# Performance work log

Hardware: AMD Instinct MI355X
Metric: run time of the kernel (lower is better)

Reference implementation:

```python
import jax, jax.numpy as jnp
import numpy as np

MARGIN = 0.5  # init kwarg 'margin'
TWO_N, D = 8192, 256


def setup_inputs() -> dict:
    key = jax.random.key(0)
    k1, k2 = jax.random.split(key)
    embeddings = jax.random.normal(k1, (TWO_N, D), dtype=jnp.float32)
    neg_mask = jax.random.bernoulli(k2, 0.5, (TWO_N, TWO_N))  # bool [2N, 2N]
    return {"embeddings": embeddings, "neg_mask": neg_mask}


def _cdist(x, y):
    # Euclidean pairwise distances via the Gram trick (matches torch.cdist p=2)
    x2 = jnp.sum(x * x, axis=-1)[:, None]
    y2 = jnp.sum(y * y, axis=-1)[None, :]
    sq = jnp.maximum(x2 + y2 - 2.0 * (x @ y.T), 0.0)
    return jnp.sqrt(sq + 1e-12)


def reference(embeddings, neg_mask):
    two_n = embeddings.shape[0]
    n = two_n // 2
    d = _cdist(embeddings, embeddings)  # [2N, 2N]
    # masked sum of exp(margin - d) per anchor row (vectorizes the python loop)
    exp_neg = jnp.where(neg_mask, jnp.exp(MARGIN - d), 0.0)
    row_sums = exp_neg.sum(axis=1)  # [2N]
    idx = jnp.arange(n)
    ap = d[idx, idx + n]  # anchor-positive distances [N]
    j = jnp.log(row_sums[:n] + row_sums[n:]) + ap  # [N]
    # original skips NaN entries before the mean
    valid = ~jnp.isnan(j)
    r2 = jnp.where(valid, jnp.square(jnp.maximum(j, 0.0)), 0.0)
    cnt = jnp.maximum(valid.sum(), 1).astype(r2.dtype)
    loss = r2.sum() / cnt / 2.0
    return loss
```

## Files before the change

### kernel.cpp

```cpp
#include <hip/hip_runtime.h>
#include <hip/hip_bf16.h>
#include <stdint.h>

#define TWO_N  8192
#define NHALF  4096
#define DDIM   256
#define MARGIN 0.5f
#define NTRI   2080

static const size_t OFF_EMB  = 0;
static const size_t OFF_X2   = 4u * 1024 * 1024;
static const size_t OFF_AP   = OFF_X2 + (size_t)TWO_N * 4;
static const size_t OFF_FLAG = OFF_AP + (size_t)NHALF * 4;
static const size_t OFF_BITM = 5u * 1024 * 1024;
static const size_t OFF_RS   = 13u * 1024 * 1024;

typedef __attribute__((ext_vector_type(8))) short bf16x8;
typedef __attribute__((ext_vector_type(4))) float f32x4;

__device__ inline ushort f2bf(float f) {
  uint32_t u = __float_as_uint(f);
  uint32_t r = (u + 0x7FFFu + ((u >> 16) & 1u)) >> 16;
  return (ushort)r;
}
__device__ inline float bf2f(ushort h) { return __uint_as_float((uint32_t)h << 16); }

__device__ inline void gload_lds4(const void* g, void* l) {
  __builtin_amdgcn_global_load_lds(
      (const __attribute__((address_space(1))) uint32_t*)(uintptr_t)g,
      (__attribute__((address_space(3))) uint32_t*)(uint32_t)(uintptr_t)l,
      4, 0, 0);
}

__global__ __launch_bounds__(256) void smv2_prep(
    const float* __restrict__ emb,
    const uint32_t* __restrict__ maskw,
    ushort* __restrict__ emb_bf,
    float* __restrict__ x2,
    int* __restrict__ flag)
{
  const int t = threadIdx.x;
  if (blockIdx.x == 0) {
    __shared__ int sflag;
    if (t == 0) sflag = 0;
    __syncthreads();
    int found = 0;
    #pragma unroll
    for (int k = 0; k < 8; ++k) {
      uint32_t w = maskw[t * 8 + k];
      if (w > 1u && (w & 0xFEFEFEFEu) == 0u) found = 1;
    }
    if (found) atomicOr(&sflag, 1);
    __syncthreads();
    if (t == 0) *flag = sflag;
  }
  const int row  = blockIdx.x * 8 + (t >> 5);
  const int lane = t & 31;
  const float* rp = emb + (size_t)row * DDIM + lane * 8;
  float4 v0 = *(const float4*)(rp);
  float4 v1 = *(const float4*)(rp + 4);
  float vals[8] = {v0.x, v0.y, v0.z, v0.w, v1.x, v1.y, v1.z, v1.w};
  uint32_t packed[4];
  float ss = 0.f;
  #pragma unroll
  for (int k = 0; k < 4; ++k) {
    ushort h0 = f2bf(vals[2 * k]);
    ushort h1 = f2bf(vals[2 * k + 1]);
    packed[k] = (uint32_t)h0 | ((uint32_t)h1 << 16);
    float f0 = bf2f(h0), f1 = bf2f(h1);
    ss += f0 * f0 + f1 * f1;
  }
  *(uint4*)(emb_bf + (size_t)row * DDIM + lane * 8) =
      make_uint4(packed[0], packed[1], packed[2], packed[3]);
  #pragma unroll
  for (int m = 1; m < 32; m <<= 1) ss += __shfl_xor(ss, m);
  if (lane == 0) x2[row] = ss;
}

__global__ __launch_bounds__(256) void smv2_pack(
    const uint8_t* __restrict__ mask8,
    const int* __restrict__ flagp,
    uint32_t* __restrict__ bitM,
    float* __restrict__ rs)
{
  const int t = threadIdx.x;
  if (blockIdx.x == 0) {
    float4 z = {0.f, 0.f, 0.f, 0.f};
    #pragma unroll
    for (int i = 0; i < 8; ++i) ((float4*)rs)[t * 8 + i] = z;
  }
  const int tid = blockIdx.x * 256 + t;
  const int isByte = *flagp;
  if (isByte) {
    #pragma unroll
    for (int it = 0; it < 4; ++it) {
      const int idx = it * (2048 * 256) + tid;
      const uint4 a = ((const uint4*)mask8)[(size_t)idx * 2];
      const uint4 b = ((const uint4*)mask8)[(size_t)idx * 2 + 1];
      const uint32_t wsv[8] = {a.x, a.y, a.z, a.w, b.x, b.y, b.z, b.w};
      uint32_t out = 0;
      #pragma unroll
      for (int j = 0; j < 8; ++j)
        out |= ((((wsv[j] & 0x01010101u) * 0x01020408u) >> 24) & 0xFu) << (4 * j);
      bitM[idx] = out;
    }
  } else {
    const uint32_t* maskw = (const uint32_t*)mask8;
    #pragma unroll
    for (int it = 0; it < 4; ++it) {
      const int idx = it * (2048 * 256) + tid;
      uint32_t out = 0;
      #pragma unroll
      for (int j = 0; j < 8; ++j) {
        const uint4 wv = ((const uint4*)maskw)[(size_t)idx * 8 + j];
        out |= (wv.x != 0u ? 1u : 0u) << (4 * j);
        out |= (wv.y != 0u ? 1u : 0u) << (4 * j + 1);
        out |= (wv.z != 0u ? 1u : 0u) << (4 * j + 2);
        out |= (wv.w != 0u ? 1u : 0u) << (4 * j + 3);
      }
      bitM[idx] = out;
    }
  }
}

__global__ __launch_bounds__(512, 6) void smv2_main(
    const ushort* __restrict__ emb_bf,
    const float* __restrict__ x2,
    const uint8_t* __restrict__ bitM,
    float* __restrict__ ap,
    float* __restrict__ rs)
{
  __shared__ uint32_t ldsM[512];
  __shared__ float ldsX[256];
  __shared__ float part[512];
  __shared__ float part2[256];

  const int t = threadIdx.x;

  const int bid = blockIdx.x;
  const int idx = (bid & 7) * (NTRI / 8) + (bid >> 3);
  float rf = sqrtf(8.f * (float)idx + 1.f);
  int bx = (int)((rf - 1.f) * 0.5f);
  while ((bx + 1) * (bx + 2) / 2 <= idx) ++bx;
  while (bx * (bx + 1) / 2 > idx) --bx;
  const int by = idx - bx * (bx + 1) / 2;
  const int brow = by * 128;
  const int bcol = bx * 128;
  const bool diag = (bx == by);

  const int w  = t >> 6;
  const int l  = t & 63;
  const int wr = w >> 2;
  const int wc = w & 3;
  const int cl = l & 15;
  const int kh = l >> 4;
  const int srow = t >> 2;

  gload_lds4(bitM + (size_t)(brow + srow) * 1024 + (bcol >> 3) + (t & 3) * 4,
             (char*)ldsM + t * 4);
  {
    const int xi = t & 255;
    const float* src = (xi < 128) ? (x2 + brow + xi) : (x2 + bcol + (xi - 128));
    gload_lds4(src, (char*)ldsX + xi * 4);
  }
  uint2 m2[2];
  #pragma unroll
  for (int n = 0; n < 2; ++n) {
    const int gj = bcol + wc * 32 + n * 16 + cl;
    m2[n] = *(const uint2*)(bitM + (size_t)gj * 1024 + (brow >> 3) + wr * 8);
  }

  const char* pA = (const char*)emb_bf + (size_t)(brow + wr * 64 + cl) * 512 + kh * 16;
  const char* pB = (const char*)emb_bf + (size_t)(bcol + wc * 32 + cl) * 512 + kh * 16;

  f32x4 acc[4][2];
  #pragma unroll
  for (int m = 0; m < 4; ++m)
    #pragma unroll
    for (int n = 0; n < 2; ++n) {
      f32x4 z = {0.f, 0.f, 0.f, 0.f};
      acc[m][n] = z;
    }

  #pragma unroll
  for (int p = 0; p < 8; ++p) {
    bf16x8 a0 = *(const bf16x8*)(pA + 0 * 8192 + p * 64);
    bf16x8 a1 = *(const bf16x8*)(pA + 1 * 8192 + p * 64);
    bf16x8 a2 = *(const bf16x8*)(pA + 2 * 8192 + p * 64);
    bf16x8 a3 = *(const bf16x8*)(pA + 3 * 8192 + p * 64);
    bf16x8 b0 = *(const bf16x8*)(pB + 0 * 8192 + p * 64);
    bf16x8 b1 = *(const bf16x8*)(pB + 1 * 8192 + p * 64);
    acc[0][0] = __builtin_amdgcn_mfma_f32_16x16x32_bf16(a0, b0, acc[0][0], 0, 0, 0);
    acc[0][1] = __builtin_amdgcn_mfma_f32_16x16x32_bf16(a0, b1, acc[0][1], 0, 0, 0);
    acc[1][0] = __builtin_amdgcn_mfma_f32_16x16x32_bf16(a1, b0, acc[1][0], 0, 0, 0);
    acc[1][1] = __builtin_amdgcn_mfma_f32_16x16x32_bf16(a1, b1, acc[1][1], 0, 0, 0);
    acc[2][0] = __builtin_amdgcn_mfma_f32_16x16x32_bf16(a2, b0, acc[2][0], 0, 0, 0);
    acc[2][1] = __builtin_amdgcn_mfma_f32_16x16x32_bf16(a2, b1, acc[2][1], 0, 0, 0);
    acc[3][0] = __builtin_amdgcn_mfma_f32_16x16x32_bf16(a3, b0, acc[3][0], 0, 0, 0);
    acc[3][1] = __builtin_amdgcn_mfma_f32_16x16x32_bf16(a3, b1, acc[3][1], 0, 0, 0);
  }

  __syncthreads();

  float cs[2] = {0.f, 0.f};

  #pragma unroll
  for (int m = 0; m < 4; ++m) {
    #pragma unroll
    for (int q = 0; q < 4; ++q) {
      const int lrow = wr * 64 + m * 16 + kh * 4 + q;
      const int gi = brow + lrow;
      const float xi = ldsX[lrow];
      const uint32_t m1w = ldsM[lrow * 4 + wc];
      float rp = 0.f;
      #pragma unroll
      for (int n = 0; n < 2; ++n) {
        const int jc = wc * 32 + n * 16 + cl;
        const int gj = bcol + jc;
        const float g = acc[m][n][q];
        float sq = (gi == gj) ? 0.f : (xi + ldsX[128 + jc] - 2.f * g);
        sq = fmaxf(sq, 0.f) + 1e-12f;
        const float dd = __builtin_amdgcn_sqrtf(sq);
        if (gj == gi + NHALF && gi < NHALF) ap[gi] = dd;
        const float e = __expf(MARGIN - dd);
        const uint32_t mk1 = (m1w >> (n * 16 + cl)) & 1u;
        rp += mk1 ? e : 0.f;
        const uint32_t m2bits = (m < 2) ? m2[n].x : m2[n].y;
        const uint32_t mk2 = (m2bits >> ((m & 1) * 16 + kh * 4 + q)) & 1u;
        cs[n] += mk2 ? e : 0.f;
      }
      #pragma unroll
      for (int s = 1; s < 16; s <<= 1) rp += __shfl_xor(rp, s);
      if (cl == 0) part[wc * 128 + lrow] = rp;
    }
  }

  #pragma unroll
  for (int n = 0; n < 2; ++n) {
    cs[n] += __shfl_xor(cs[n], 16);
    cs[n] += __shfl_xor(cs[n], 32);
    if (l < 16) part2[wr * 128 + wc * 32 + n * 16 + l] = cs[n];
  }
  __syncthreads();

  if (t < 128) {
    atomicAdd(&rs[brow + t],
              (part[t] + part[128 + t]) + (part[256 + t] + part[384 + t]));
    if (!diag)
      atomicAdd(&rs[bcol + t], part2[t] + part2[128 + t]);
  }
}

__global__ __launch_bounds__(1024) void smv2_finalize(
    const float* __restrict__ rs, const float* __restrict__ ap,
    float* __restrict__ out)
{
  const int t = threadIdx.x;
  float sum = 0.f, cnt = 0.f;
  for (int i = t; i < NHALF; i += 1024) {
    float rsum = rs[i] + rs[i + NHALF];
    float jv = logf(rsum) + ap[i];
    if (!isnan(jv)) {
      cnt += 1.f;
      float mj = fmaxf(jv, 0.f);
      sum += mj * mj;
    }
  }
  __shared__ float ssum[16], scnt[16];
  #pragma unroll
  for (int s = 32; s >= 1; s >>= 1) {
    sum += __shfl_down(sum, s);
    cnt += __shfl_down(cnt, s);
  }
  const int wid = t >> 6, lid = t & 63;
  if (lid == 0) { ssum[wid] = sum; scnt[wid] = cnt; }
  __syncthreads();
  if (t == 0) {
    float S = 0.f, C = 0.f;
    #pragma unroll
    for (int i = 0; i < 16; ++i) { S += ssum[i]; C += scnt[i]; }
    if (C < 1.f) C = 1.f;
    out[0] = S / C * 0.5f;
  }
}

extern "C" void kernel_launch(void* const* d_in, const int* in_sizes, int n_in,
                              void* d_out, int out_size, void* d_ws, size_t ws_size,
                              hipStream_t stream) {
  const float* emb = (const float*)d_in[0];
  const void* mask = d_in[1];
  char* ws = (char*)d_ws;

  ushort*   emb_bf = (ushort*)(ws + OFF_EMB);
  float*    x2     = (float*)(ws + OFF_X2);
  float*    ap     = (float*)(ws + OFF_AP);
  int*      flag   = (int*)(ws + OFF_FLAG);
  uint32_t* bitM   = (uint32_t*)(ws + OFF_BITM);
  float*    rs     = (float*)(ws + OFF_RS);

  smv2_prep<<<1024, 256, 0, stream>>>(emb, (const uint32_t*)mask, emb_bf, x2, flag);
  smv2_pack<<<2048, 256, 0, stream>>>((const uint8_t*)mask, flag, bitM, rs);
  smv2_main<<<NTRI, 512, 0, stream>>>(emb_bf, x2, (const uint8_t*)bitM, ap, rs);
  smv2_finalize<<<1, 1024, 0, stream>>>(rs, ap, (float*)d_out);
}
```

Before: 490.3 us.

## Replace triangular tile grid with row-strip blocks streaming B through double-buffered LDS

The main kernel drops the symmetric upper-triangle 128x128 tiling with atomics. Each block now owns 32 full rows, keeps its A fragments in registers, and streams all 8192 columns of B through double-buffered, XOR-swizzled LDS using 16-byte global_load_lds. Row sums are written directly instead of atomically, so the rs zeroing in pack is removed. This gives up the symmetry saving (about twice the MFMA and exp work) and launches only 256 blocks, in exchange for no atomics, fewer global mask reads and pipelined loads.

```diff
diff --git a/kernel.cpp b/kernel.cpp
--- a/kernel.cpp
+++ b/kernel.cpp
@@ -6,7 +6,6 @@
 #define NHALF  4096
 #define DDIM   256
 #define MARGIN 0.5f
-#define NTRI   2080
 
 static const size_t OFF_EMB  = 0;
 static const size_t OFF_X2   = 4u * 1024 * 1024;
@@ -25,12 +24,15 @@
 }
 __device__ inline float bf2f(ushort h) { return __uint_as_float((uint32_t)h << 16); }
 
-__device__ inline void gload_lds4(const void* g, void* l) {
+__device__ inline void gload_lds16(const void* g, void* l) {
   __builtin_amdgcn_global_load_lds(
       (const __attribute__((address_space(1))) uint32_t*)(uintptr_t)g,
       (__attribute__((address_space(3))) uint32_t*)(uint32_t)(uintptr_t)l,
-      4, 0, 0);
-}
+      16, 0, 0);
+}
+
+#define STR2(x) #x
+#define WAITVM(N) asm volatile("s_waitcnt vmcnt(" STR2(N) ")" ::: "memory")
 
 __global__ __launch_bounds__(256) void smv2_prep(
     const float* __restrict__ emb,
@@ -80,15 +82,9 @@
 __global__ __launch_bounds__(256) void smv2_pack(
     const uint8_t* __restrict__ mask8,
     const int* __restrict__ flagp,
-    uint32_t* __restrict__ bitM,
-    float* __restrict__ rs)
+    uint32_t* __restrict__ bitM)
 {
   const int t = threadIdx.x;
-  if (blockIdx.x == 0) {
-    float4 z = {0.f, 0.f, 0.f, 0.f};
-    #pragma unroll
-    for (int i = 0; i < 8; ++i) ((float4*)rs)[t * 8 + i] = z;
-  }
   const int tid = blockIdx.x * 256 + t;
   const int isByte = *flagp;
   if (isByte) {
@@ -123,132 +119,155 @@
   }
 }
 
-__global__ __launch_bounds__(512, 6) void smv2_main(
+__global__ __launch_bounds__(512, 4) void smv2_main(
     const ushort* __restrict__ emb_bf,
     const float* __restrict__ x2,
-    const uint8_t* __restrict__ bitM,
+    const uint32_t* __restrict__ bitM,
     float* __restrict__ ap,
     float* __restrict__ rs)
 {
-  __shared__ uint32_t ldsM[512];
-  __shared__ float ldsX[256];
-  __shared__ float part[512];
-  __shared__ float part2[256];
+  __shared__ char bufB[2][32768];
+  __shared__ uint32_t ldsM[32 * 256];
+  __shared__ float ldsX[TWO_N];
+  __shared__ float pRed[2][16][4];
 
   const int t = threadIdx.x;
-
-  const int bid = blockIdx.x;
-  const int idx = (bid & 7) * (NTRI / 8) + (bid >> 3);
-  float rf = sqrtf(8.f * (float)idx + 1.f);
-  int bx = (int)((rf - 1.f) * 0.5f);
-  while ((bx + 1) * (bx + 2) / 2 <= idx) ++bx;
-  while (bx * (bx + 1) / 2 > idx) --bx;
-  const int by = idx - bx * (bx + 1) / 2;
-  const int brow = by * 128;
-  const int bcol = bx * 128;
-  const bool diag = (bx == by);
-
-  const int w  = t >> 6;
-  const int l  = t & 63;
-  const int wr = w >> 2;
-  const int wc = w & 3;
-  const int cl = l & 15;
-  const int kh = l >> 4;
-  const int srow = t >> 2;
-
-  gload_lds4(bitM + (size_t)(brow + srow) * 1024 + (bcol >> 3) + (t & 3) * 4,
-             (char*)ldsM + t * 4);
-  {
-    const int xi = t & 255;
-    const float* src = (xi < 128) ? (x2 + brow + xi) : (x2 + bcol + (xi - 128));
-    gload_lds4(src, (char*)ldsX + xi * 4);
-  }
-  uint2 m2[2];
-  #pragma unroll
-  for (int n = 0; n < 2; ++n) {
-    const int gj = bcol + wc * 32 + n * 16 + cl;
-    m2[n] = *(const uint2*)(bitM + (size_t)gj * 1024 + (brow >> 3) + wr * 8);
-  }
-
-  const char* pA = (const char*)emb_bf + (size_t)(brow + wr * 64 + cl) * 512 + kh * 16;
-  const char* pB = (const char*)emb_bf + (size_t)(bcol + wc * 32 + cl) * 512 + kh * 16;
-
-  f32x4 acc[4][2];
-  #pragma unroll
-  for (int m = 0; m < 4; ++m)
-    #pragma unroll
-    for (int n = 0; n < 2; ++n) {
-      f32x4 z = {0.f, 0.f, 0.f, 0.f};
-      acc[m][n] = z;
-    }
-
-  #pragma unroll
-  for (int p = 0; p < 8; ++p) {
-    bf16x8 a0 = *(const bf16x8*)(pA + 0 * 8192 + p * 64);
-    bf16x8 a1 = *(const bf16x8*)(pA + 1 * 8192 + p * 64);
-    bf16x8 a2 = *(const bf16x8*)(pA + 2 * 8192 + p * 64);
-    bf16x8 a3 = *(const bf16x8*)(pA + 3 * 8192 + p * 64);
-    bf16x8 b0 = *(const bf16x8*)(pB + 0 * 8192 + p * 64);
-    bf16x8 b1 = *(const bf16x8*)(pB + 1 * 8192 + p * 64);
-    acc[0][0] = __builtin_amdgcn_mfma_f32_16x16x32_bf16(a0, b0, acc[0][0], 0, 0, 0);
-    acc[0][1] = __builtin_amdgcn_mfma_f32_16x16x32_bf16(a0, b1, acc[0][1], 0, 0, 0);
-    acc[1][0] = __builtin_amdgcn_mfma_f32_16x16x32_bf16(a1, b0, acc[1][0], 0, 0, 0);
-    acc[1][1] = __builtin_amdgcn_mfma_f32_16x16x32_bf16(a1, b1, acc[1][1], 0, 0, 0);
-    acc[2][0] = __builtin_amdgcn_mfma_f32_16x16x32_bf16(a2, b0, acc[2][0], 0, 0, 0);
-    acc[2][1] = __builtin_amdgcn_mfma_f32_16x16x32_bf16(a2, b1, acc[2][1], 0, 0, 0);
-    acc[3][0] = __builtin_amdgcn_mfma_f32_16x16x32_bf16(a3, b0, acc[3][0], 0, 0, 0);
-    acc[3][1] = __builtin_amdgcn_mfma_f32_16x16x32_bf16(a3, b1, acc[3][1], 0, 0, 0);
-  }
-
+  const int brow = blockIdx.x * 32;
+
+  const int w   = t >> 6;
+  const int l   = t & 63;
+  const int wr2 = w >> 2;
+  const int wcb = w & 3;
+  const int cl  = l & 15;
+  const int kh  = l >> 4;
+
+  const int srowb = w * 8 + (l >> 5);
+  const int scolb = (l & 31) * 16;
+  const int wl16  = w * 4096 + l * 16;
+
+#define STAGEP(GP, BUFI)                                                    \
+  {                                                                         \
+    _Pragma("unroll")                                                       \
+    for (int i_ = 0; i_ < 4; ++i_) {                                        \
+      const int row_ = srowb + i_ * 2;                                      \
+      gload_lds16((GP) + (size_t)row_ * 512 + (scolb ^ ((row_ & 7) << 4)),  \
+                  bufB[BUFI] + wl16 + i_ * 1024);                           \
+    }                                                                       \
+  }
+
+  const char* pA = (const char*)emb_bf + (size_t)(brow + wr2 * 16 + cl) * 512 + kh * 16;
+  bf16x8 afr[8];
+  #pragma unroll
+  for (int ks = 0; ks < 8; ++ks) afr[ks] = *(const bf16x8*)(pA + (size_t)ks * 64);
+
+  #pragma unroll
+  for (int i = 0; i < 4; ++i)
+    gload_lds16((const char*)bitM + (size_t)brow * 1024 + wl16 + i * 1024,
+                (char*)ldsM + wl16 + i * 1024);
+  #pragma unroll
+  for (int i = 0; i < 4; ++i)
+    gload_lds16((const char*)x2 + wl16 + i * 1024, (char*)ldsX + wl16 + i * 1024);
+  STAGEP((const char*)emb_bf, 0);
+
+  const int bswz = (cl & 7) << 4;
+  const int brow512 = (wcb * 16 + cl) * 512;
+
+#define COMPUTE(BUFI, ACC)                                                  \
+  {                                                                         \
+    const char* bb = bufB[BUFI] + brow512;                                  \
+    f32x4 a_ = {0.f, 0.f, 0.f, 0.f};                                        \
+    _Pragma("unroll")                                                       \
+    for (int ks = 0; ks < 8; ++ks) {                                        \
+      bf16x8 bfr = *(const bf16x8*)(bb + (((ks * 64) | (kh * 16)) ^ bswz)); \
+      a_ = __builtin_amdgcn_mfma_f32_16x16x32_bf16(afr[ks], bfr, a_, 0, 0, 0); \
+    }                                                                       \
+    ACC = a_;                                                               \
+  }
+
+  float rsum0 = 0.f, rsum1 = 0.f, rsum2 = 0.f, rsum3 = 0.f;
+  float xi0, xi1, xi2, xi3;
+  const int rl0 = wr2 * 16 + kh * 4;
+
+#define EPI(ACC, COLG)                                                      \
+  {                                                                         \
+    const float xj = ldsX[COLG];                                            \
+    _Pragma("unroll")                                                       \
+    for (int q = 0; q < 4; ++q) {                                           \
+      const int rg = brow + rl0 + q;                                        \
+      const float xiq = (q == 0) ? xi0 : (q == 1) ? xi1 : (q == 2) ? xi2 : xi3; \
+      const float g = (ACC)[q];                                             \
+      float sq = (rg == (COLG)) ? 0.f : (xiq + xj - 2.f * g);               \
+      sq = fmaxf(sq, 0.f) + 1e-12f;                                         \
+      const float dd = __builtin_amdgcn_sqrtf(sq);                          \
+      if ((COLG) == rg + NHALF) ap[rg] = dd;                                \
+      const uint32_t mk = (ldsM[(rl0 + q) * 256 + ((COLG) >> 5)] >> ((COLG) & 31)) & 1u; \
+      const float e = mk ? __expf(MARGIN - dd) : 0.f;                       \
+      if (q == 0) rsum0 += e; else if (q == 1) rsum1 += e;                  \
+      else if (q == 2) rsum2 += e; else rsum3 += e;                         \
+    }                                                                       \
+  }
+
+  f32x4 acc;
+  const char* gNext = (const char*)emb_bf + 32768;
+  int colg = wcb * 16 + cl;
+
+  STAGEP(gNext, 1); gNext += 32768;
+  __builtin_amdgcn_sched_barrier(0);
+  WAITVM(4);
+  __builtin_amdgcn_s_barrier();
+  __builtin_amdgcn_sched_barrier(0);
+  xi0 = ldsX[brow + rl0 + 0]; xi1 = ldsX[brow + rl0 + 1];
+  xi2 = ldsX[brow + rl0 + 2]; xi3 = ldsX[brow + rl0 + 3];
+  COMPUTE(0, acc);
+  EPI(acc, colg);
+  colg += 64;
+
+  for (int it = 0; it < 63; ++it) {
+    STAGEP(gNext, 0); gNext += 32768;
+    __builtin_amdgcn_sched_barrier(0);
+    WAITVM(4);
+    __builtin_amdgcn_s_barrier();
+    __builtin_amdgcn_sched_barrier(0);
+    COMPUTE(1, acc);
+    EPI(acc, colg);
+    colg += 64;
+    STAGEP(gNext, 1); gNext += 32768;
+    __builtin_amdgcn_sched_barrier(0);
+    WAITVM(4);
+    __builtin_amdgcn_s_barrier();
+    __builtin_amdgcn_sched_barrier(0);
+    COMPUTE(0, acc);
+    EPI(acc, colg);
+    colg += 64;
+  }
+
+  WAITVM(0);
+  __builtin_amdgcn_s_barrier();
+  __builtin_amdgcn_sched_barrier(0);
+  COMPUTE(1, acc);
+  EPI(acc, colg);
+
+  #pragma unroll
+  for (int s = 1; s < 16; s <<= 1) {
+    rsum0 += __shfl_xor(rsum0, s);
+    rsum1 += __shfl_xor(rsum1, s);
+    rsum2 += __shfl_xor(rsum2, s);
+    rsum3 += __shfl_xor(rsum3, s);
+  }
+  if (cl == 0) {
+    pRed[wr2][kh * 4 + 0][wcb] = rsum0;
+    pRed[wr2][kh * 4 + 1][wcb] = rsum1;
+    pRed[wr2][kh * 4 + 2][wcb] = rsum2;
+    pRed[wr2][kh * 4 + 3][wcb] = rsum3;
+  }
   __syncthreads();
-
-  float cs[2] = {0.f, 0.f};
-
-  #pragma unroll
-  for (int m = 0; m < 4; ++m) {
-    #pragma unroll
-    for (int q = 0; q < 4; ++q) {
-      const int lrow = wr * 64 + m * 16 + kh * 4 + q;
-      const int gi = brow + lrow;
-      const float xi = ldsX[lrow];
-      const uint32_t m1w = ldsM[lrow * 4 + wc];
-      float rp = 0.f;
-      #pragma unroll
-      for (int n = 0; n < 2; ++n) {
-        const int jc = wc * 32 + n * 16 + cl;
-        const int gj = bcol + jc;
-        const float g = acc[m][n][q];
-        float sq = (gi == gj) ? 0.f : (xi + ldsX[128 + jc] - 2.f * g);
-        sq = fmaxf(sq, 0.f) + 1e-12f;
-        const float dd = __builtin_amdgcn_sqrtf(sq);
-        if (gj == gi + NHALF && gi < NHALF) ap[gi] = dd;
-        const float e = __expf(MARGIN - dd);
-        const uint32_t mk1 = (m1w >> (n * 16 + cl)) & 1u;
-        rp += mk1 ? e : 0.f;
-        const uint32_t m2bits = (m < 2) ? m2[n].x : m2[n].y;
-        const uint32_t mk2 = (m2bits >> ((m & 1) * 16 + kh * 4 + q)) & 1u;
-        cs[n] += mk2 ? e : 0.f;
-      }
-      #pragma unroll
-      for (int s = 1; s < 16; s <<= 1) rp += __shfl_xor(rp, s);
-      if (cl == 0) part[wc * 128 + lrow] = rp;
-    }
-  }
-
-  #pragma unroll
-  for (int n = 0; n < 2; ++n) {
-    cs[n] += __shfl_xor(cs[n], 16);
-    cs[n] += __shfl_xor(cs[n], 32);
-    if (l < 16) part2[wr * 128 + wc * 32 + n * 16 + l] = cs[n];
-  }
-  __syncthreads();
-
-  if (t < 128) {
-    atomicAdd(&rs[brow + t],
-              (part[t] + part[128 + t]) + (part[256 + t] + part[384 + t]));
-    if (!diag)
-      atomicAdd(&rs[bcol + t], part2[t] + part2[128 + t]);
-  }
+  if (t < 32) {
+    const float* p = pRed[t >> 4][t & 15];
+    rs[brow + t] = (p[0] + p[1]) + (p[2] + p[3]);
+  }
+#undef EPI
+#undef COMPUTE
+#undef STAGEP
 }
 
 __global__ __launch_bounds__(1024) void smv2_finalize(
@@ -299,7 +318,7 @@
   float*    rs     = (float*)(ws + OFF_RS);
 
   smv2_prep<<<1024, 256, 0, stream>>>(emb, (const uint32_t*)mask, emb_bf, x2, flag);
-  smv2_pack<<<2048, 256, 0, stream>>>((const uint8_t*)mask, flag, bitM, rs);
-  smv2_main<<<NTRI, 512, 0, stream>>>(emb_bf, x2, (const uint8_t*)bitM, ap, rs);
+  smv2_pack<<<2048, 256, 0, stream>>>((const uint8_t*)mask, flag, bitM);
+  smv2_main<<<256, 512, 0, stream>>>(emb_bf, x2, bitM, ap, rs);
   smv2_finalize<<<1, 1024, 0, stream>>>(rs, ap, (float*)d_out);
 }
```

Result: faster. 478.4 us (-2.4%).
